# Optimization experiments

Hardware: AMD Instinct MI355X
Metric: run time of the kernel (lower is better)

## Reference

```python
import jax, jax.numpy as jnp
import numpy as np

C = 256
C8 = C // 8


def setup_inputs() -> dict:
    key = jax.random.key(0)
    ks = jax.random.split(key, 9)
    B, H, W = 4, 64, 64
    s = 1.0 / np.sqrt(C)
    return {
        "pre_feat": jax.random.normal(ks[0], (B, C, H, W), jnp.float32),
        "post_feat": jax.random.normal(ks[1], (B, C, H, W), jnp.float32),
        "Wq": jax.random.normal(ks[2], (C8, C), jnp.float32) * s,
        "bq": jnp.zeros((C8,), jnp.float32),
        "Wk": jax.random.normal(ks[3], (C8, C), jnp.float32) * s,
        "bk": jnp.zeros((C8,), jnp.float32),
        "Wv": jax.random.normal(ks[4], (C, C), jnp.float32) * s,
        "bv": jnp.zeros((C,), jnp.float32),
        "gamma": jnp.zeros((1,), jnp.float32),
    }


def reference(pre_feat, post_feat, Wq, bq, Wk, bk, Wv, bv, gamma):
    B, Cc, H, W = pre_feat.shape
    N = H * W
    pre = pre_feat.reshape(B, Cc, N)    # (B, C, N)
    post = post_feat.reshape(B, Cc, N)
    # 1x1 convs == per-pixel linear projections
    q = jnp.einsum('dc,bcn->bdn', Wq, post) + bq[None, :, None]  # (B, C8, N)
    k = jnp.einsum('dc,bcn->bdn', Wk, pre) + bk[None, :, None]   # (B, C8, N)
    v = jnp.einsum('dc,bcn->bdn', Wv, pre) + bv[None, :, None]   # (B, C, N)
    # energy[b,i,j] = <q[b,:,i], k[b,:,j]>  (unscaled)
    energy = jnp.einsum('bdi,bdj->bij', q, k)                    # (B, N, N)
    attention = jax.nn.softmax(energy, axis=-1)
    # out[b,c,i] = sum_j v[b,c,j] * attention[b,i,j]
    out = jnp.einsum('bcj,bij->bci', v, attention).reshape(B, Cc, H, W)
    return gamma[0] * out + post_feat
```

## Files before the change

### kernel.cpp

```cpp
#include <hip/hip_runtime.h>
#include <hip/hip_bf16.h>

#define Bn 4
#define Cn 256
#define Dn 32
#define Nn 4096

typedef __bf16 bf16x8 __attribute__((ext_vector_type(8)));
typedef float f32x4 __attribute__((ext_vector_type(4)));

__device__ __forceinline__ float bf2f(unsigned short u) {
  unsigned int v = ((unsigned int)u) << 16;
  return __builtin_bit_cast(float, v);
}
__device__ __forceinline__ unsigned short f2bf(float f) {
  unsigned int v = __builtin_bit_cast(unsigned int, f);
  v += 0x7FFFu + ((v >> 16) & 1u);
  return (unsigned short)(v >> 16);
}
__device__ __forceinline__ unsigned int pk2(float a, float b) {
  union { __hip_bfloat162 h; unsigned int u; } x;
  x.h = __float22bfloat162_rn(make_float2(a, b));
  return x.u;
}
__device__ __forceinline__ bf16x8 ldfrag(const unsigned short* p) {
  return __builtin_bit_cast(bf16x8, *(const uint4*)p);
}
__device__ __forceinline__ uint4 pack8(const float* p) {
  float4 a = *(const float4*)p;
  float4 b = *(const float4*)(p + 4);
  union { unsigned int u2[4]; uint4 u; } x;
  x.u2[0] = pk2(a.x, a.y); x.u2[1] = pk2(a.z, a.w);
  x.u2[2] = pk2(b.x, b.y); x.u2[3] = pk2(b.z, b.w);
  return x.u;
}
__device__ __forceinline__ void async16(unsigned short* lds, const unsigned short* g) {
  __builtin_amdgcn_global_load_lds(
      (const __attribute__((address_space(1))) unsigned int*)g,
      (__attribute__((address_space(3))) unsigned int*)lds, 16, 0, 0);
}

__global__ __launch_bounds__(256) void wconv(
    const float* __restrict__ Wq, const float* __restrict__ Wk,
    const float* __restrict__ Wv,
    unsigned short* __restrict__ WqBf, unsigned short* __restrict__ WkBf,
    unsigned short* __restrict__ WvBf)
{
  const size_t base = ((size_t)blockIdx.x * 256 + threadIdx.x) * 8;
  if (base < 8192) {
    *(uint4*)(WqBf + base) = pack8(Wq + base);
  } else if (base < 16384) {
    *(uint4*)(WkBf + base - 8192) = pack8(Wk + base - 8192);
  } else {
    *(uint4*)(WvBf + base - 16384) = pack8(Wv + base - 16384);
  }
}

__global__ __launch_bounds__(256) void qkprep(
    const float* __restrict__ pre, const float* __restrict__ post,
    const unsigned short* __restrict__ WqBf, const float* __restrict__ bq,
    const unsigned short* __restrict__ WkBf, const float* __restrict__ bk,
    const unsigned short* __restrict__ WvBf, const float* __restrict__ bv,
    unsigned short* __restrict__ Qt, unsigned short* __restrict__ Kt,
    unsigned short* __restrict__ VBf)
{
  __shared__ __align__(16) unsigned short sV[256 * 40];

  const int tid = threadIdx.x;
  const int lane = tid & 63, w = tid >> 6;
  const int quad = lane >> 4, n16 = lane & 15;
  const int b = blockIdx.x >> 7;
  const int i0 = (blockIdx.x & 127) << 5;
  const int isub = w & 1, dh = w >> 1;
  const int i = i0 + isub * 16 + n16;

  const f32x4 zz = {0.f, 0.f, 0.f, 0.f};
  f32x4 aq = zz, ak = zz;
  f32x4 accv[8];
#pragma unroll
  for (int ct = 0; ct < 8; ct++) accv[ct] = zz;

  const float* postB = post + (size_t)b * Cn * Nn + i;
  const float* preB  = pre  + (size_t)b * Cn * Nn + i;

#pragma unroll
  for (int kc = 0; kc < 8; kc++) {
    const int c0 = kc * 32 + quad * 8;
    const float* pp = postB + (size_t)c0 * Nn;
    const float* pr = preB + (size_t)c0 * Nn;
    union { unsigned int u2[4]; bf16x8 v; } bp, bq8;
#pragma unroll
    for (int e2 = 0; e2 < 4; e2++) {
      float p0 = pp[(size_t)(2 * e2) * Nn], p1 = pp[(size_t)(2 * e2 + 1) * Nn];
      float r0 = pr[(size_t)(2 * e2) * Nn], r1 = pr[(size_t)(2 * e2 + 1) * Nn];
      bp.u2[e2] = pk2(p0, p1);
      bq8.u2[e2] = pk2(r0, r1);
    }
    bf16x8 awq = ldfrag(WqBf + (size_t)(dh * 16 + n16) * Cn + kc * 32 + quad * 8);
    bf16x8 awk = ldfrag(WkBf + (size_t)(dh * 16 + n16) * Cn + kc * 32 + quad * 8);
    aq = __builtin_amdgcn_mfma_f32_16x16x32_bf16(awq, bp.v, aq, 0, 0, 0);
    ak = __builtin_amdgcn_mfma_f32_16x16x32_bf16(awk, bq8.v, ak, 0, 0, 0);
#pragma unroll
    for (int ct = 0; ct < 8; ct++) {
      bf16x8 aw = ldfrag(WvBf + (size_t)(dh * 128 + ct * 16 + n16) * Cn + kc * 32 + quad * 8);
      accv[ct] = __builtin_amdgcn_mfma_f32_16x16x32_bf16(aw, bq8.v, accv[ct], 0, 0, 0);
    }
  }

  const float LOG2E = 1.44269504f;
  union { unsigned short s[4]; uint2 u; } oq, ok;
#pragma unroll
  for (int r = 0; r < 4; r++) {
    int d = dh * 16 + quad * 4 + r;
    oq.s[r] = f2bf((aq[r] + bq[d]) * LOG2E);
    ok.s[r] = f2bf(ak[r] + bk[d]);
  }
  *(uint2*)(Qt + ((size_t)b * Nn + i) * Dn + dh * 16 + quad * 4) = oq.u;
  *(uint2*)(Kt + ((size_t)b * Nn + i) * Dn + dh * 16 + quad * 4) = ok.u;

#pragma unroll
  for (int ct = 0; ct < 8; ct++) {
#pragma unroll
    for (int r = 0; r < 4; r++) {
      const int c = dh * 128 + ct * 16 + quad * 4 + r;
      sV[c * 40 + isub * 16 + n16] = f2bf(accv[ct][r] + bv[c]);
    }
  }
  __syncthreads();
#pragma unroll
  for (int k = 0; k < 4; k++) {
    const int slot = tid + k * 256;
    const int c = slot >> 2, seg = slot & 3;
    *(uint4*)(VBf + ((size_t)b * Cn + c) * Nn + i0 + seg * 8) =
        *(const uint4*)(sV + c * 40 + seg * 8);
  }
}

__global__ __launch_bounds__(256, 4) void flash_attn(
    const unsigned short* __restrict__ Qt, const unsigned short* __restrict__ Kt,
    const unsigned short* __restrict__ VBf,
    unsigned short* __restrict__ Opart, float* __restrict__ Lpart)
{
  __shared__ __align__(16) unsigned short sX[256 * 64];
  __shared__ __align__(16) unsigned short Pl[64 * 64];

  const int tid = threadIdx.x;
  const int lane = tid & 63, w = tid >> 6;
  const int quad = lane >> 4, n16 = lane & 15;
  const int bid = blockIdx.x;
  const int pair = bid & 7, sub = bid >> 3;
  const int b  = pair >> 1;
  const int js = ((pair & 1) << 1) | (sub >> 6);
  const int it = sub & 63;
  const int i0 = it * 64;
  const int jbase = js * 1024;

  const bf16x8 qf = ldfrag(Qt + ((size_t)b * Nn + i0 + w * 16 + n16) * Dn + quad * 8);

  const f32x4 zz = {0.f, 0.f, 0.f, 0.f};
  f32x4 acc[4][4];
#pragma unroll
  for (int sub2 = 0; sub2 < 4; sub2++)
#pragma unroll
    for (int ct = 0; ct < 4; ct++) acc[sub2][ct] = zz;
  float lrow = 0.f;

  const size_t laneoff = (size_t)(lane >> 3) * Nn + (size_t)(((lane & 7) ^ (lane >> 3)) << 3);
  const unsigned short* preB = VBf + (size_t)b * Cn * Nn + laneoff;
  const int xsw = n16 & 7;
  const int xoff0 = (quad ^ xsw) << 3;
  const int xoff1 = ((4 + quad) ^ xsw) << 3;
  const int psw = (n16 & 7) << 3;

  for (int t = 0; t < 16; ++t) {
    const int j0 = jbase + t * 64;
    __syncthreads();
#pragma unroll
    for (int k = 0; k < 8; k++) {
      const int rb = (k * 4 + w) * 8;
      async16(sX + rb * 64 + (lane << 3), preB + (size_t)rb * Nn + j0);
    }
    {
      f32x4 sc[4];
#pragma unroll
      for (int jt = 0; jt < 4; jt++) {
        bf16x8 akf = ldfrag(Kt + ((size_t)b * Nn + j0 + jt * 16 + n16) * Dn + quad * 8);
        sc[jt] = __builtin_amdgcn_mfma_f32_16x16x32_bf16(akf, qf, zz, 0, 0, 0);
      }
      float ps = 0.f;
#pragma unroll
      for (int jt = 0; jt < 4; jt++) {
        float p0 = exp2f(fminf(sc[jt][0], 101.f));
        float p1 = exp2f(fminf(sc[jt][1], 101.f));
        float p2 = exp2f(fminf(sc[jt][2], 101.f));
        float p3 = exp2f(fminf(sc[jt][3], 101.f));
        ps += (p0 + p1) + (p2 + p3);
        union { unsigned int u2[2]; uint2 u; } pk;
        pk.u2[0] = pk2(p0, p1);
        pk.u2[1] = pk2(p2, p3);
        *(uint2*)&Pl[(size_t)(w * 16 + n16) * 64 + ((jt * 16 + quad * 4) ^ psw)] = pk.u;
      }
      ps += __shfl_xor(ps, 16);
      ps += __shfl_xor(ps, 32);
      lrow += ps;
    }
    __syncthreads();

    __builtin_amdgcn_s_setprio(1);
#pragma unroll
    for (int kc = 0; kc < 2; kc++) {
      const int xo = kc ? xoff1 : xoff0;
      bf16x8 pB[4];
#pragma unroll
      for (int sub2 = 0; sub2 < 4; sub2++)
        pB[sub2] = ldfrag(&Pl[(size_t)(sub2 * 16 + n16) * 64 + ((kc * 32 + quad * 8) ^ psw)]);
#pragma unroll
      for (int ct = 0; ct < 4; ct++) {
        const int crow = w * 64 + ct * 16 + n16;
        bf16x8 av = ldfrag(&sX[crow * 64 + xo]);
        acc[0][ct] = __builtin_amdgcn_mfma_f32_16x16x32_bf16(av, pB[0], acc[0][ct], 0, 0, 0);
        acc[1][ct] = __builtin_amdgcn_mfma_f32_16x16x32_bf16(av, pB[1], acc[1][ct], 0, 0, 0);
        acc[2][ct] = __builtin_amdgcn_mfma_f32_16x16x32_bf16(av, pB[2], acc[2][ct], 0, 0, 0);
        acc[3][ct] = __builtin_amdgcn_mfma_f32_16x16x32_bf16(av, pB[3], acc[3][ct], 0, 0, 0);
      }
    }
    __builtin_amdgcn_s_setprio(0);
  }

  const size_t pbase = (size_t)(js * 4 + b) * Nn;
  if (quad == 0) Lpart[pbase + i0 + w * 16 + n16] = lrow;
#pragma unroll
  for (int sub2 = 0; sub2 < 4; sub2++) {
    const int i = i0 + sub2 * 16 + n16;
#pragma unroll
    for (int ct = 0; ct < 4; ct++) {
      union { unsigned int u2[2]; uint2 u; } pk;
      pk.u2[0] = pk2(acc[sub2][ct][0], acc[sub2][ct][1]);
      pk.u2[1] = pk2(acc[sub2][ct][2], acc[sub2][ct][3]);
      *(uint2*)(Opart + (pbase + i) * 256 + w * 64 + ct * 16 + quad * 4) = pk.u;
    }
  }
}

__global__ __launch_bounds__(256) void combine(
    const unsigned short* __restrict__ Opart, const float* __restrict__ Lpart,
    const float* __restrict__ post, const float* __restrict__ gamma,
    float* __restrict__ out)
{
  __shared__ float sT[64 * 65];
  __shared__ float sL[64];

  const int tid = threadIdx.x;
  const int b = blockIdx.x >> 8;
  const int rest = blockIdx.x & 255;
  const int i0 = (rest >> 2) * 64;
  const int c0 = (rest & 3) * 64;

  if (tid < 64) {
    float l = 0.f;
#pragma unroll
    for (int js = 0; js < 4; js++) l += Lpart[(size_t)(js * 4 + b) * Nn + i0 + tid];
    sL[tid] = 1.f / l;
  }
  __syncthreads();

#pragma unroll
  for (int pass = 0; pass < 2; pass++) {
    const int il = (tid >> 3) + pass * 32;
    const int c8 = (tid & 7) << 3;
    float a[8] = {0.f, 0.f, 0.f, 0.f, 0.f, 0.f, 0.f, 0.f};
#pragma unroll
    for (int js = 0; js < 4; js++) {
      uint4 uu = *(const uint4*)(Opart + ((size_t)(js * 4 + b) * Nn + i0 + il) * 256 + c0 + c8);
      const unsigned short* us = (const unsigned short*)&uu;
#pragma unroll
      for (int e = 0; e < 8; e++) a[e] += bf2f(us[e]);
    }
    const float inv = sL[il];
#pragma unroll
    for (int e = 0; e < 8; e++) sT[(c8 + e) * 65 + il] = a[e] * inv;
  }
  __syncthreads();

  const float g = gamma[0];
#pragma unroll
  for (int itr = 0; itr < 4; itr++) {
    const int slot = tid + itr * 256;
    const int cr = slot >> 4, i4 = (slot & 15) << 2;
    const size_t addr = ((size_t)b * Cn + c0 + cr) * Nn + i0 + i4;
    float4 pp = *(const float4*)(post + addr);
    float4 ov;
    ov.x = g * sT[cr * 65 + i4 + 0] + pp.x;
    ov.y = g * sT[cr * 65 + i4 + 1] + pp.y;
    ov.z = g * sT[cr * 65 + i4 + 2] + pp.z;
    ov.w = g * sT[cr * 65 + i4 + 3] + pp.w;
    *(float4*)(out + addr) = ov;
  }
}

extern "C" void kernel_launch(void* const* d_in, const int* in_sizes, int n_in,
                              void* d_out, int out_size, void* d_ws, size_t ws_size,
                              hipStream_t stream) {
  const float* pre   = (const float*)d_in[0];
  const float* post  = (const float*)d_in[1];
  const float* Wq    = (const float*)d_in[2];
  const float* bq    = (const float*)d_in[3];
  const float* Wk    = (const float*)d_in[4];
  const float* bk    = (const float*)d_in[5];
  const float* Wv    = (const float*)d_in[6];
  const float* bv    = (const float*)d_in[7];
  const float* gamma = (const float*)d_in[8];
  float* out = (float*)d_out;

  unsigned short* ws = (unsigned short*)d_ws;
  unsigned short* Qt    = ws;
  unsigned short* Kt    = Qt + (size_t)Bn * Nn * Dn;
  unsigned short* VBf   = Kt + (size_t)Bn * Nn * Dn;
  unsigned short* WqBf  = VBf + (size_t)Bn * Cn * Nn;
  unsigned short* WkBf  = WqBf + Dn * Cn;
  unsigned short* WvBf  = WkBf + Dn * Cn;
  float* Lpart = (float*)(WvBf + Cn * Cn);
  unsigned short* Opart = (unsigned short*)(Lpart + 4 * Bn * Nn);

  wconv<<<40, 256, 0, stream>>>(Wq, Wk, Wv, WqBf, WkBf, WvBf);
  qkprep<<<512, 256, 0, stream>>>(pre, post, WqBf, bq, WkBf, bk, WvBf, bv,
                                  Qt, Kt, VBf);
  flash_attn<<<1024, 256, 0, stream>>>(Qt, Kt, VBf, Opart, Lpart);
  combine<<<1024, 256, 0, stream>>>(Opart, Lpart, post, gamma, out);
}
```

Measured before the change: 183.2 us.

## Repartition qkprep to 16-pixel blocks with per-wave channel split

The projection kernel now processes 16 pixels per block instead of 32 and launches 1024 blocks. Each wave computes a 64-channel slice of V, while wave 0 alone computes Q and wave 1 alone computes K, so the pre/post features are loaded less redundantly per wave. This raises block count for better occupancy and load spread, at the cost of reading each weight matrix twice as often across blocks and uneven work between waves. The shared staging buffer shrinks accordingly.

```diff
diff --git a/kernel.cpp b/kernel.cpp
--- a/kernel.cpp
+++ b/kernel.cpp
@@ -64,21 +64,21 @@
     unsigned short* __restrict__ Qt, unsigned short* __restrict__ Kt,
     unsigned short* __restrict__ VBf)
 {
-  __shared__ __align__(16) unsigned short sV[256 * 40];
+  __shared__ __align__(16) unsigned short sV[256 * 24];
 
   const int tid = threadIdx.x;
   const int lane = tid & 63, w = tid >> 6;
   const int quad = lane >> 4, n16 = lane & 15;
-  const int b = blockIdx.x >> 7;
-  const int i0 = (blockIdx.x & 127) << 5;
-  const int isub = w & 1, dh = w >> 1;
-  const int i = i0 + isub * 16 + n16;
+  const int b = blockIdx.x >> 8;
+  const int i0 = (blockIdx.x & 255) << 4;
+  const int i = i0 + n16;
+  const int cbase = w * 64;
 
   const f32x4 zz = {0.f, 0.f, 0.f, 0.f};
-  f32x4 aq = zz, ak = zz;
-  f32x4 accv[8];
-#pragma unroll
-  for (int ct = 0; ct < 8; ct++) accv[ct] = zz;
+  f32x4 accv[4];
+#pragma unroll
+  for (int ct = 0; ct < 4; ct++) accv[ct] = zz;
+  f32x4 aqk0 = zz, aqk1 = zz;
 
   const float* postB = post + (size_t)b * Cn * Nn + i;
   const float* preB  = pre  + (size_t)b * Cn * Nn + i;
@@ -86,53 +86,76 @@
 #pragma unroll
   for (int kc = 0; kc < 8; kc++) {
     const int c0 = kc * 32 + quad * 8;
-    const float* pp = postB + (size_t)c0 * Nn;
     const float* pr = preB + (size_t)c0 * Nn;
-    union { unsigned int u2[4]; bf16x8 v; } bp, bq8;
+    union { unsigned int u2[4]; bf16x8 v; } bq8;
 #pragma unroll
     for (int e2 = 0; e2 < 4; e2++) {
-      float p0 = pp[(size_t)(2 * e2) * Nn], p1 = pp[(size_t)(2 * e2 + 1) * Nn];
       float r0 = pr[(size_t)(2 * e2) * Nn], r1 = pr[(size_t)(2 * e2 + 1) * Nn];
-      bp.u2[e2] = pk2(p0, p1);
       bq8.u2[e2] = pk2(r0, r1);
     }
-    bf16x8 awq = ldfrag(WqBf + (size_t)(dh * 16 + n16) * Cn + kc * 32 + quad * 8);
-    bf16x8 awk = ldfrag(WkBf + (size_t)(dh * 16 + n16) * Cn + kc * 32 + quad * 8);
-    aq = __builtin_amdgcn_mfma_f32_16x16x32_bf16(awq, bp.v, aq, 0, 0, 0);
-    ak = __builtin_amdgcn_mfma_f32_16x16x32_bf16(awk, bq8.v, ak, 0, 0, 0);
-#pragma unroll
-    for (int ct = 0; ct < 8; ct++) {
-      bf16x8 aw = ldfrag(WvBf + (size_t)(dh * 128 + ct * 16 + n16) * Cn + kc * 32 + quad * 8);
+    if (w == 0) {
+      const float* pp = postB + (size_t)c0 * Nn;
+      union { unsigned int u2[4]; bf16x8 v; } bp;
+#pragma unroll
+      for (int e2 = 0; e2 < 4; e2++) {
+        float p0 = pp[(size_t)(2 * e2) * Nn], p1 = pp[(size_t)(2 * e2 + 1) * Nn];
+        bp.u2[e2] = pk2(p0, p1);
+      }
+      bf16x8 awq0 = ldfrag(WqBf + (size_t)(n16) * Cn + kc * 32 + quad * 8);
+      bf16x8 awq1 = ldfrag(WqBf + (size_t)(16 + n16) * Cn + kc * 32 + quad * 8);
+      aqk0 = __builtin_amdgcn_mfma_f32_16x16x32_bf16(awq0, bp.v, aqk0, 0, 0, 0);
+      aqk1 = __builtin_amdgcn_mfma_f32_16x16x32_bf16(awq1, bp.v, aqk1, 0, 0, 0);
+    } else if (w == 1) {
+      bf16x8 awk0 = ldfrag(WkBf + (size_t)(n16) * Cn + kc * 32 + quad * 8);
+      bf16x8 awk1 = ldfrag(WkBf + (size_t)(16 + n16) * Cn + kc * 32 + quad * 8);
+      aqk0 = __builtin_amdgcn_mfma_f32_16x16x32_bf16(awk0, bq8.v, aqk0, 0, 0, 0);
+      aqk1 = __builtin_amdgcn_mfma_f32_16x16x32_bf16(awk1, bq8.v, aqk1, 0, 0, 0);
+    }
+#pragma unroll
+    for (int ct = 0; ct < 4; ct++) {
+      bf16x8 aw = ldfrag(WvBf + (size_t)(cbase + ct * 16 + n16) * Cn + kc * 32 + quad * 8);
       accv[ct] = __builtin_amdgcn_mfma_f32_16x16x32_bf16(aw, bq8.v, accv[ct], 0, 0, 0);
     }
   }
 
   const float LOG2E = 1.44269504f;
-  union { unsigned short s[4]; uint2 u; } oq, ok;
-#pragma unroll
-  for (int r = 0; r < 4; r++) {
-    int d = dh * 16 + quad * 4 + r;
-    oq.s[r] = f2bf((aq[r] + bq[d]) * LOG2E);
-    ok.s[r] = f2bf(ak[r] + bk[d]);
-  }
-  *(uint2*)(Qt + ((size_t)b * Nn + i) * Dn + dh * 16 + quad * 4) = oq.u;
-  *(uint2*)(Kt + ((size_t)b * Nn + i) * Dn + dh * 16 + quad * 4) = ok.u;
-
-#pragma unroll
-  for (int ct = 0; ct < 8; ct++) {
+  if (w == 0) {
+#pragma unroll
+    for (int dh = 0; dh < 2; dh++) {
+      const f32x4 a = dh ? aqk1 : aqk0;
+      union { unsigned short s[4]; uint2 u; } oq;
+#pragma unroll
+      for (int r = 0; r < 4; r++)
+        oq.s[r] = f2bf((a[r] + bq[dh * 16 + quad * 4 + r]) * LOG2E);
+      *(uint2*)(Qt + ((size_t)b * Nn + i) * Dn + dh * 16 + quad * 4) = oq.u;
+    }
+  } else if (w == 1) {
+#pragma unroll
+    for (int dh = 0; dh < 2; dh++) {
+      const f32x4 a = dh ? aqk1 : aqk0;
+      union { unsigned short s[4]; uint2 u; } ok;
+#pragma unroll
+      for (int r = 0; r < 4; r++)
+        ok.s[r] = f2bf(a[r] + bk[dh * 16 + quad * 4 + r]);
+      *(uint2*)(Kt + ((size_t)b * Nn + i) * Dn + dh * 16 + quad * 4) = ok.u;
+    }
+  }
+
+#pragma unroll
+  for (int ct = 0; ct < 4; ct++) {
 #pragma unroll
     for (int r = 0; r < 4; r++) {
-      const int c = dh * 128 + ct * 16 + quad * 4 + r;
-      sV[c * 40 + isub * 16 + n16] = f2bf(accv[ct][r] + bv[c]);
+      const int c = cbase + ct * 16 + quad * 4 + r;
+      sV[c * 24 + n16] = f2bf(accv[ct][r] + bv[c]);
     }
   }
   __syncthreads();
 #pragma unroll
-  for (int k = 0; k < 4; k++) {
-    const int slot = tid + k * 256;
-    const int c = slot >> 2, seg = slot & 3;
-    *(uint4*)(VBf + ((size_t)b * Cn + c) * Nn + i0 + seg * 8) =
-        *(const uint4*)(sV + c * 40 + seg * 8);
+  for (int pass = 0; pass < 2; pass++) {
+    const int slot = tid + pass * 256;
+    const int c = slot >> 1, half = slot & 1;
+    *(uint4*)(VBf + ((size_t)b * Cn + c) * Nn + i0 + half * 8) =
+        *(const uint4*)(sV + c * 24 + half * 8);
   }
 }
 
@@ -323,8 +346,8 @@
   unsigned short* Opart = (unsigned short*)(Lpart + 4 * Bn * Nn);
 
   wconv<<<40, 256, 0, stream>>>(Wq, Wk, Wv, WqBf, WkBf, WvBf);
-  qkprep<<<512, 256, 0, stream>>>(pre, post, WqBf, bq, WkBf, bk, WvBf, bv,
-                                  Qt, Kt, VBf);
+  qkprep<<<1024, 256, 0, stream>>>(pre, post, WqBf, bq, WkBf, bk, WvBf, bv,
+                                   Qt, Kt, VBf);
   flash_attn<<<1024, 256, 0, stream>>>(Qt, Kt, VBf, Opart, Lpart);
   combine<<<1024, 256, 0, stream>>>(Opart, Lpart, post, gamma, out);
 }
```

Result: slower. 190.5 us (+4.0%).

## Pre-transpose pre/post features to bf16 pixel-major layout before projection

Applied to the files above, without the earlier changes.

Adds a prep kernel that transposes pre and post feature maps through LDS into bf16 [B,N,C] buffers, folded into the same launch as the weight conversion. qkprep then loads 16-byte contiguous fragments instead of doing strided scalar fp32 loads across channels and packing them in registers. This costs an extra full read/write pass over both feature tensors and reuses the Opart workspace region as scratch before flash_attn overwrites it.

```diff
diff --git a/kernel.cpp b/kernel.cpp
--- a/kernel.cpp
+++ b/kernel.cpp
@@ -40,24 +40,58 @@
       (__attribute__((address_space(3))) unsigned int*)lds, 16, 0, 0);
 }
 
-__global__ __launch_bounds__(256) void wconv(
+__global__ __launch_bounds__(256) void prep(
+    const float* __restrict__ pre, const float* __restrict__ post,
     const float* __restrict__ Wq, const float* __restrict__ Wk,
     const float* __restrict__ Wv,
+    unsigned short* __restrict__ preT, unsigned short* __restrict__ postT,
     unsigned short* __restrict__ WqBf, unsigned short* __restrict__ WkBf,
     unsigned short* __restrict__ WvBf)
 {
-  const size_t base = ((size_t)blockIdx.x * 256 + threadIdx.x) * 8;
-  if (base < 8192) {
-    *(uint4*)(WqBf + base) = pack8(Wq + base);
-  } else if (base < 16384) {
-    *(uint4*)(WkBf + base - 8192) = pack8(Wk + base - 8192);
-  } else {
-    *(uint4*)(WvBf + base - 16384) = pack8(Wv + base - 16384);
+  const int blk = blockIdx.x, tid = threadIdx.x;
+  if (blk >= 2048) {
+    const size_t base = ((size_t)(blk - 2048) * 256 + tid) * 8;
+    if (base < 8192) {
+      *(uint4*)(WqBf + base) = pack8(Wq + base);
+    } else if (base < 16384) {
+      *(uint4*)(WkBf + base - 8192) = pack8(Wk + base - 8192);
+    } else {
+      *(uint4*)(WvBf + base - 16384) = pack8(Wv + base - 16384);
+    }
+    return;
+  }
+  __shared__ float tile[64 * 65];
+  const float* src = (blk < 1024) ? pre : post;
+  unsigned short* dst = (blk < 1024) ? preT : postT;
+  const int q = blk & 1023;
+  const int b = q >> 8, ct = (q >> 6) & 3, nt = q & 63;
+
+  const int cr = tid >> 4;
+  const int nc4 = (tid & 15) << 2;
+#pragma unroll
+  for (int k = 0; k < 4; k++) {
+    const int c = cr + k * 16;
+    float4 v = *(const float4*)(src + ((size_t)(b * Cn + ct * 64 + c)) * Nn + nt * 64 + nc4);
+    tile[c * 65 + nc4 + 0] = v.x;
+    tile[c * 65 + nc4 + 1] = v.y;
+    tile[c * 65 + nc4 + 2] = v.z;
+    tile[c * 65 + nc4 + 3] = v.w;
+  }
+  __syncthreads();
+#pragma unroll
+  for (int p = 0; p < 2; p++) {
+    const int s = tid + p * 256;
+    const int nr = s >> 3, c8 = (s & 7) << 3;
+    union { unsigned int u2[4]; uint4 u; } pk;
+#pragma unroll
+    for (int e2 = 0; e2 < 4; e2++)
+      pk.u2[e2] = pk2(tile[(c8 + 2 * e2) * 65 + nr], tile[(c8 + 2 * e2 + 1) * 65 + nr]);
+    *(uint4*)(dst + ((size_t)(b * Nn + nt * 64 + nr)) * Cn + ct * 64 + c8) = pk.u;
   }
 }
 
 __global__ __launch_bounds__(256) void qkprep(
-    const float* __restrict__ pre, const float* __restrict__ post,
+    const unsigned short* __restrict__ preT, const unsigned short* __restrict__ postT,
     const unsigned short* __restrict__ WqBf, const float* __restrict__ bq,
     const unsigned short* __restrict__ WkBf, const float* __restrict__ bk,
     const unsigned short* __restrict__ WvBf, const float* __restrict__ bv,
@@ -80,30 +114,22 @@
 #pragma unroll
   for (int ct = 0; ct < 8; ct++) accv[ct] = zz;
 
-  const float* postB = post + (size_t)b * Cn * Nn + i;
-  const float* preB  = pre  + (size_t)b * Cn * Nn + i;
+  const unsigned short* preTb  = preT  + ((size_t)b * Nn + i) * Cn;
+  const unsigned short* postTb = postT + ((size_t)b * Nn + i) * Cn;
 
 #pragma unroll
   for (int kc = 0; kc < 8; kc++) {
-    const int c0 = kc * 32 + quad * 8;
-    const float* pp = postB + (size_t)c0 * Nn;
-    const float* pr = preB + (size_t)c0 * Nn;
-    union { unsigned int u2[4]; bf16x8 v; } bp, bq8;
-#pragma unroll
-    for (int e2 = 0; e2 < 4; e2++) {
-      float p0 = pp[(size_t)(2 * e2) * Nn], p1 = pp[(size_t)(2 * e2 + 1) * Nn];
-      float r0 = pr[(size_t)(2 * e2) * Nn], r1 = pr[(size_t)(2 * e2 + 1) * Nn];
-      bp.u2[e2] = pk2(p0, p1);
-      bq8.u2[e2] = pk2(r0, r1);
-    }
-    bf16x8 awq = ldfrag(WqBf + (size_t)(dh * 16 + n16) * Cn + kc * 32 + quad * 8);
-    bf16x8 awk = ldfrag(WkBf + (size_t)(dh * 16 + n16) * Cn + kc * 32 + quad * 8);
-    aq = __builtin_amdgcn_mfma_f32_16x16x32_bf16(awq, bp.v, aq, 0, 0, 0);
-    ak = __builtin_amdgcn_mfma_f32_16x16x32_bf16(awk, bq8.v, ak, 0, 0, 0);
+    const int co = kc * 32 + quad * 8;
+    bf16x8 bp  = ldfrag(postTb + co);
+    bf16x8 bq8 = ldfrag(preTb + co);
+    bf16x8 awq = ldfrag(WqBf + (size_t)(dh * 16 + n16) * Cn + co);
+    bf16x8 awk = ldfrag(WkBf + (size_t)(dh * 16 + n16) * Cn + co);
+    aq = __builtin_amdgcn_mfma_f32_16x16x32_bf16(awq, bp, aq, 0, 0, 0);
+    ak = __builtin_amdgcn_mfma_f32_16x16x32_bf16(awk, bq8, ak, 0, 0, 0);
 #pragma unroll
     for (int ct = 0; ct < 8; ct++) {
-      bf16x8 aw = ldfrag(WvBf + (size_t)(dh * 128 + ct * 16 + n16) * Cn + kc * 32 + quad * 8);
-      accv[ct] = __builtin_amdgcn_mfma_f32_16x16x32_bf16(aw, bq8.v, accv[ct], 0, 0, 0);
+      bf16x8 aw = ldfrag(WvBf + (size_t)(dh * 128 + ct * 16 + n16) * Cn + co);
+      accv[ct] = __builtin_amdgcn_mfma_f32_16x16x32_bf16(aw, bq8, accv[ct], 0, 0, 0);
     }
   }
 
@@ -321,9 +347,12 @@
   unsigned short* WvBf  = WkBf + Dn * Cn;
   float* Lpart = (float*)(WvBf + Cn * Cn);
   unsigned short* Opart = (unsigned short*)(Lpart + 4 * Bn * Nn);
-
-  wconv<<<40, 256, 0, stream>>>(Wq, Wk, Wv, WqBf, WkBf, WvBf);
-  qkprep<<<512, 256, 0, stream>>>(pre, post, WqBf, bq, WkBf, bk, WvBf, bv,
+  unsigned short* preT  = Opart;
+  unsigned short* postT = Opart + (size_t)Bn * Nn * Cn;
+
+  prep<<<2088, 256, 0, stream>>>(pre, post, Wq, Wk, Wv,
+                                 preT, postT, WqBf, WkBf, WvBf);
+  qkprep<<<512, 256, 0, stream>>>(preT, postT, WqBf, bq, WkBf, bk, WvBf, bv,
                                   Qt, Kt, VBf);
   flash_attn<<<1024, 256, 0, stream>>>(Qt, Kt, VBf, Opart, Lpart);
   combine<<<1024, 256, 0, stream>>>(Opart, Lpart, post, gamma, out);
```

New measurement: 185.4 us. No clear change (+1.2%).

## Fuse split-KV combine into flash_attn via last-arriver atomic ticket

Applied to the files above, without the earlier changes.

Removes the separate combine kernel. Each flash_attn block increments a per-(batch, query-tile) counter after writing its partial output. The fourth (last) block to arrive reduces the four partials, normalizes them, and writes gamma*out+post. This saves a kernel launch and the inter-kernel gap, and lets the combine overlap with other attention blocks. The cost is serialized combine work in the last-arriving blocks, plus fences and atomics, and the counter is reset inside the wconv kernel.

```diff
diff --git a/kernel.cpp b/kernel.cpp
--- a/kernel.cpp
+++ b/kernel.cpp
@@ -44,8 +44,9 @@
     const float* __restrict__ Wq, const float* __restrict__ Wk,
     const float* __restrict__ Wv,
     unsigned short* __restrict__ WqBf, unsigned short* __restrict__ WkBf,
-    unsigned short* __restrict__ WvBf)
+    unsigned short* __restrict__ WvBf, unsigned int* __restrict__ cnt)
 {
+  if (blockIdx.x == 0) cnt[threadIdx.x] = 0u;
   const size_t base = ((size_t)blockIdx.x * 256 + threadIdx.x) * 8;
   if (base < 8192) {
     *(uint4*)(WqBf + base) = pack8(Wq + base);
@@ -139,7 +140,9 @@
 __global__ __launch_bounds__(256, 4) void flash_attn(
     const unsigned short* __restrict__ Qt, const unsigned short* __restrict__ Kt,
     const unsigned short* __restrict__ VBf,
-    unsigned short* __restrict__ Opart, float* __restrict__ Lpart)
+    unsigned short* __restrict__ Opart, float* __restrict__ Lpart,
+    const float* __restrict__ post, const float* __restrict__ gamma,
+    float* __restrict__ out, unsigned int* __restrict__ cnt)
 {
   __shared__ __align__(16) unsigned short sX[256 * 64];
   __shared__ __align__(16) unsigned short Pl[64 * 64];
@@ -240,61 +243,61 @@
       *(uint2*)(Opart + (pbase + i) * 256 + w * 64 + ct * 16 + quad * 4) = pk.u;
     }
   }
-}
-
-__global__ __launch_bounds__(256) void combine(
-    const unsigned short* __restrict__ Opart, const float* __restrict__ Lpart,
-    const float* __restrict__ post, const float* __restrict__ gamma,
-    float* __restrict__ out)
-{
-  __shared__ float sT[64 * 65];
-  __shared__ float sL[64];
-
-  const int tid = threadIdx.x;
-  const int b = blockIdx.x >> 8;
-  const int rest = blockIdx.x & 255;
-  const int i0 = (rest >> 2) * 64;
-  const int c0 = (rest & 3) * 64;
-
-  if (tid < 64) {
-    float l = 0.f;
-#pragma unroll
-    for (int js = 0; js < 4; js++) l += Lpart[(size_t)(js * 4 + b) * Nn + i0 + tid];
-    sL[tid] = 1.f / l;
-  }
+
   __syncthreads();
-
-#pragma unroll
-  for (int pass = 0; pass < 2; pass++) {
-    const int il = (tid >> 3) + pass * 32;
-    const int c8 = (tid & 7) << 3;
-    float a[8] = {0.f, 0.f, 0.f, 0.f, 0.f, 0.f, 0.f, 0.f};
-#pragma unroll
-    for (int js = 0; js < 4; js++) {
-      uint4 uu = *(const uint4*)(Opart + ((size_t)(js * 4 + b) * Nn + i0 + il) * 256 + c0 + c8);
-      const unsigned short* us = (const unsigned short*)&uu;
-#pragma unroll
-      for (int e = 0; e < 8; e++) a[e] += bf2f(us[e]);
-    }
-    const float inv = sL[il];
-#pragma unroll
-    for (int e = 0; e < 8; e++) sT[(c8 + e) * 65 + il] = a[e] * inv;
+  int* tktp = (int*)Pl;
+  if (tid == 0) {
+    __threadfence();
+    *tktp = (int)atomicAdd(&cnt[b * 64 + it], 1u);
   }
   __syncthreads();
-
-  const float g = gamma[0];
-#pragma unroll
-  for (int itr = 0; itr < 4; itr++) {
-    const int slot = tid + itr * 256;
-    const int cr = slot >> 4, i4 = (slot & 15) << 2;
-    const size_t addr = ((size_t)b * Cn + c0 + cr) * Nn + i0 + i4;
-    float4 pp = *(const float4*)(post + addr);
-    float4 ov;
-    ov.x = g * sT[cr * 65 + i4 + 0] + pp.x;
-    ov.y = g * sT[cr * 65 + i4 + 1] + pp.y;
-    ov.z = g * sT[cr * 65 + i4 + 2] + pp.z;
-    ov.w = g * sT[cr * 65 + i4 + 3] + pp.w;
-    *(float4*)(out + addr) = ov;
+  if (*tktp == 3) {
+    __threadfence();
+    float* sT = (float*)sX;
+    float* sL = (float*)(Pl + 16);
+    if (tid < 64) {
+      float l = 0.f;
+#pragma unroll
+      for (int j2 = 0; j2 < 4; j2++) l += Lpart[(size_t)(j2 * 4 + b) * Nn + i0 + tid];
+      sL[tid] = 1.f / l;
+    }
+    __syncthreads();
+    const float g = gamma[0];
+#pragma unroll
+    for (int cq = 0; cq < 4; cq++) {
+      const int c0 = cq * 64;
+#pragma unroll
+      for (int pass = 0; pass < 2; pass++) {
+        const int il = (tid >> 3) + pass * 32;
+        const int c8 = (tid & 7) << 3;
+        float a[8] = {0.f, 0.f, 0.f, 0.f, 0.f, 0.f, 0.f, 0.f};
+#pragma unroll
+        for (int j2 = 0; j2 < 4; j2++) {
+          uint4 uu = *(const uint4*)(Opart + ((size_t)(j2 * 4 + b) * Nn + i0 + il) * 256 + c0 + c8);
+          const unsigned short* us = (const unsigned short*)&uu;
+#pragma unroll
+          for (int e = 0; e < 8; e++) a[e] += bf2f(us[e]);
+        }
+        const float inv = sL[il];
+#pragma unroll
+        for (int e = 0; e < 8; e++) sT[(c8 + e) * 65 + il] = a[e] * inv;
+      }
+      __syncthreads();
+#pragma unroll
+      for (int itr = 0; itr < 4; itr++) {
+        const int slot = tid + itr * 256;
+        const int cr = slot >> 4, i4 = (slot & 15) << 2;
+        const size_t addr = ((size_t)b * Cn + c0 + cr) * Nn + i0 + i4;
+        float4 pp = *(const float4*)(post + addr);
+        float4 ov;
+        ov.x = g * sT[cr * 65 + i4 + 0] + pp.x;
+        ov.y = g * sT[cr * 65 + i4 + 1] + pp.y;
+        ov.z = g * sT[cr * 65 + i4 + 2] + pp.z;
+        ov.w = g * sT[cr * 65 + i4 + 3] + pp.w;
+        *(float4*)(out + addr) = ov;
+      }
+      __syncthreads();
+    }
   }
 }
 
@@ -321,10 +324,11 @@
   unsigned short* WvBf  = WkBf + Dn * Cn;
   float* Lpart = (float*)(WvBf + Cn * Cn);
   unsigned short* Opart = (unsigned short*)(Lpart + 4 * Bn * Nn);
-
-  wconv<<<40, 256, 0, stream>>>(Wq, Wk, Wv, WqBf, WkBf, WvBf);
+  unsigned int* cnt = (unsigned int*)(Opart + (size_t)16 * Nn * 256);
+
+  wconv<<<40, 256, 0, stream>>>(Wq, Wk, Wv, WqBf, WkBf, WvBf, cnt);
   qkprep<<<512, 256, 0, stream>>>(pre, post, WqBf, bq, WkBf, bk, WvBf, bv,
                                   Qt, Kt, VBf);
-  flash_attn<<<1024, 256, 0, stream>>>(Qt, Kt, VBf, Opart, Lpart);
-  combine<<<1024, 256, 0, stream>>>(Opart, Lpart, post, gamma, out);
-}
+  flash_attn<<<1024, 256, 0, stream>>>(Qt, Kt, VBf, Opart, Lpart,
+                                       post, gamma, out, cnt);
+}
```

Result: slower. 276.0 us (+50.7%).
